# Kernel optimization log

Hardware: AMD Instinct MI355X
Metric: run time of the kernel (lower is better)

Reference implementation:

```python
import jax, jax.numpy as jnp
import numpy as np

L, D, H, W = 4, 256, 8, 20      # num_layers, hidden_dim, num_heads, walk_length
G, NPG = 512, 128               # graphs, nodes per graph (equal-size -> dense batch is a reshape)
N = G * NPG                     # 65536 nodes
E = 8 * N                       # 524288 edges (avg degree 8)
DH = D // H                     # head dim 32
FF = 2 * D                      # GPSConv MLP hidden (Linear(D, 2D))
AV, BV = 128, 8                 # padded atom / bond vocab sizes (OGB-style encoders)


def setup_inputs() -> dict:
    key = jax.random.key(0)
    ks = iter(jax.random.split(key, 40))
    nrm = lambda *s: jax.random.normal(next(ks), s, jnp.float32) * 0.02
    zeros = lambda *s: jnp.zeros(s, jnp.float32)
    ones = lambda *s: jnp.ones(s, jnp.float32)
    return dict(
        x=jax.random.randint(next(ks), (N, 9), 0, 2),
        edge_index=jax.random.randint(next(ks), (2, E), 0, N),
        edge_attr=jax.random.randint(next(ks), (E, 3), 0, 2),
        batch=jnp.repeat(jnp.arange(G), NPG),
        pe=jax.random.normal(next(ks), (N, W), jnp.float32),
        atom_emb=nrm(9, AV, D), bond_emb=nrm(3, BV, D),
        pe_w=nrm(W, D), pe_b=zeros(D),
        gine_w1=nrm(L, D, D), gine_b1=zeros(L, D),
        gine_g1=ones(L, D), gine_be1=zeros(L, D),
        gine_w2=nrm(L, D, D), gine_b2=zeros(L, D),
        attn_wqkv=nrm(L, D, 3 * D), attn_bqkv=zeros(L, 3 * D),
        attn_wo=nrm(L, D, D), attn_bo=zeros(L, D),
        n1_g=ones(L, D), n1_b=zeros(L, D),
        n2_g=ones(L, D), n2_b=zeros(L, D),
        n3_g=ones(L, D), n3_b=zeros(L, D),
        mlp_w1=nrm(L, D, FF), mlp_b1=zeros(L, FF),
        mlp_w2=nrm(L, FF, D), mlp_b2=zeros(L, D),
    )


def _bn(z, g, b):
    # BatchNorm1d over the node axis (training-mode batch statistics)
    mu = z.mean(0)
    var = z.var(0)
    return (z - mu) * jax.lax.rsqrt(var + 1e-5) * g + b


def _forward(x, edge_index, edge_attr, batch, pe, atom_emb, bond_emb, pe_w, pe_b,
             gine_w1, gine_b1, gine_g1, gine_be1, gine_w2, gine_b2,
             attn_wqkv, attn_bqkv, attn_wo, attn_bo,
             n1_g, n1_b, n2_g, n2_b, n3_g, n3_b,
             mlp_w1, mlp_b1, mlp_w2, mlp_b2):
    # AtomEncoder / BondEncoder: sum of per-column embeddings; PE fusion
    h = atom_emb[jnp.arange(9), x].sum(1) + pe @ pe_w + pe_b      # [N, D]
    ea = bond_emb[jnp.arange(3), edge_attr].sum(1)                # [E, D]
    src, dst = edge_index[0], edge_index[1]
    for l in range(L):
        # --- GINEConv: gather -> relu(x_j + e) -> scatter-add -> MLP ---
        m = jax.nn.relu(h[src] + ea)                              # [E, D]
        agg = jax.ops.segment_sum(m, dst, num_segments=N)         # [N, D]
        z = h + agg                                               # eps = 0
        z = jax.nn.relu(_bn(z @ gine_w1[l] + gine_b1[l], gine_g1[l], gine_be1[l]))
        z = jax.nn.relu(z @ gine_w2[l] + gine_b2[l])
        h_local = _bn(z + h, n1_g[l], n1_b[l])                    # residual + norm1 (dropout off)
        # --- global multi-head self-attention per graph (dense batch) ---
        xd = h.reshape(G, NPG, D)
        qkv = xd @ attn_wqkv[l] + attn_bqkv[l]                    # [G, NPG, 3D]
        q, k, v = jnp.split(qkv, 3, axis=-1)
        q = q.reshape(G, NPG, H, DH).transpose(0, 2, 1, 3)        # [G, H, NPG, DH]
        k = k.reshape(G, NPG, H, DH).transpose(0, 2, 1, 3)
        v = v.reshape(G, NPG, H, DH).transpose(0, 2, 1, 3)
        scores = jnp.einsum('ghnd,ghmd->ghnm', q, k) / jnp.sqrt(jnp.float32(DH))
        attn = jax.nn.softmax(scores, axis=-1)                    # all nodes valid (equal-size graphs)
        o = jnp.einsum('ghnm,ghmd->ghnd', attn, v)
        o = o.transpose(0, 2, 1, 3).reshape(G, NPG, D) @ attn_wo[l] + attn_bo[l]
        h_attn = _bn(o.reshape(N, D) + h, n2_g[l], n2_b[l])       # residual + norm2
        # --- combine + feed-forward MLP + norm3 ---
        out = h_local + h_attn
        out = jax.nn.relu(out @ mlp_w1[l] + mlp_b1[l]) @ mlp_w2[l] + mlp_b2[l]
        h = _bn(out, n3_g[l], n3_b[l])
    return jax.ops.segment_sum(h, batch, num_segments=G)          # global_add_pool [G, D]


def reference(x, edge_index, edge_attr, batch, pe, atom_emb, bond_emb, pe_w, pe_b,
              gine_w1, gine_b1, gine_g1, gine_be1, gine_w2, gine_b2,
              attn_wqkv, attn_bqkv, attn_wo, attn_bo,
              n1_g, n1_b, n2_g, n2_b, n3_g, n3_b,
              mlp_w1, mlp_b1, mlp_w2, mlp_b2):
    return _forward(x, edge_index, edge_attr, batch, pe, atom_emb, bond_emb, pe_w, pe_b,
                    gine_w1, gine_b1, gine_g1, gine_be1, gine_w2, gine_b2,
                    attn_wqkv, attn_bqkv, attn_wo, attn_bo,
                    n1_g, n1_b, n2_g, n2_b, n3_g, n3_b,
                    mlp_w1, mlp_b1, mlp_w2, mlp_b2)
```

## Files before the change

kernel.cpp:

```cpp
#include <hip/hip_runtime.h>
#include <stdint.h>


#define NN   65536
#define EE   524288
#define DD   256
#define LL   4
#define GG   512
#define NPGx 128
#define FFF  512

typedef __attribute__((ext_vector_type(8))) short short8;
typedef __attribute__((ext_vector_type(8))) __bf16 bf16x8;
typedef __attribute__((ext_vector_type(4))) float f32x4;

__device__ __forceinline__ float b2f(unsigned short u){
  union {unsigned int i; float f;} z; z.i = ((unsigned int)u) << 16; return z.f;
}
__device__ __forceinline__ unsigned short f2b(float f){
  union {float f; unsigned int i;} z; z.f = f;
  unsigned int r = z.i + 0x7fff + ((z.i >> 16) & 1u);
  return (unsigned short)(r >> 16);
}

__device__ __forceinline__ void gld16(void* lds, const void* g){
  __builtin_amdgcn_global_load_lds(
      (const __attribute__((address_space(1))) void*)g,
      (__attribute__((address_space(3))) void*)lds, 16, 0, 0);
}


__global__ __launch_bounds__(256) void combo_k(const float* __restrict__ be,
                                               unsigned short* __restrict__ tab){
  int c = blockIdx.x, d = threadIdx.x;
  int a0 = c & 7, a1 = (c >> 3) & 7, a2 = (c >> 6) & 7;
  tab[c*DD + d] = f2b(be[a0*DD + d] + be[(8 + a1)*DD + d] + be[(16 + a2)*DD + d]);
}

__global__ __launch_bounds__(256) void hist_k(const int* __restrict__ ei,
                                              int* __restrict__ cnt){
  for (int i = blockIdx.x*256 + threadIdx.x; i < EE; i += gridDim.x*256)
    atomicAdd(&cnt[ei[EE + i]], 1);
}

__global__ __launch_bounds__(1024) void scan_k(int* __restrict__ cnt,
                                               int* __restrict__ row_ptr){
  __shared__ int sd[1024];
  __shared__ int carry;
  int t = threadIdx.x;
  if (t == 0) carry = 0;
  __syncthreads();
  for (int base = 0; base < NN; base += 4096){
    int idx = base + t*4;
    int v0 = cnt[idx+0], v1 = cnt[idx+1], v2 = cnt[idx+2], v3 = cnt[idx+3];
    int s = v0 + v1 + v2 + v3;
    sd[t] = s; __syncthreads();
    for (int offd = 1; offd < 1024; offd <<= 1){
      int xv = (t >= offd) ? sd[t - offd] : 0;
      __syncthreads();
      sd[t] += xv;
      __syncthreads();
    }
    int excl = sd[t] - s + carry;
    row_ptr[idx+0] = excl;             cnt[idx+0] = excl;
    row_ptr[idx+1] = excl + v0;        cnt[idx+1] = excl + v0;
    row_ptr[idx+2] = excl + v0 + v1;   cnt[idx+2] = excl + v0 + v1;
    row_ptr[idx+3] = excl + v0+v1+v2;  cnt[idx+3] = excl + v0+v1+v2;
    __syncthreads();
    if (t == 0) carry += sd[1023];
    __syncthreads();
  }
  if (t == 0) row_ptr[NN] = carry;
}

__global__ __launch_bounds__(256) void fill_k(const int* __restrict__ ei,
                                              const int* __restrict__ ea,
                                              int* __restrict__ cursor,
                                              int* __restrict__ slot){
  for (int i = blockIdx.x*256 + threadIdx.x; i < EE; i += gridDim.x*256){
    int s  = ei[i];
    int dn = ei[EE + i];
    int a0 = ea[i*3+0], a1 = ea[i*3+1], a2 = ea[i*3+2];
    int cb = a0 | (a1 << 3) | (a2 << 6);
    int p = atomicAdd(&cursor[dn], 1);
    slot[p] = s | (cb << 16);
  }
}

__global__ __launch_bounds__(256) void twt_k(const float* __restrict__ w1,
                                             const float* __restrict__ w2,
                                             const float* __restrict__ wqkv,
                                             const float* __restrict__ wo,
                                             const float* __restrict__ m1,
                                             const float* __restrict__ m2,
                                             unsigned short* __restrict__ wt){
  int l = blockIdx.x / 2304;
  int r = blockIdx.x % 2304;
  const float* src; unsigned short* dst; int K, Nsrc, n;
  unsigned short* wl = wt + (size_t)l*655360;
  if (r < 256)      { src = w1  +(size_t)l*65536;  dst = wl;          K=256; Nsrc=256; n=r; }
  else if (r < 512) { src = w2  +(size_t)l*65536;  dst = wl+65536;    K=256; Nsrc=256; n=r-256; }
  else if (r < 1280){ src = wqkv+(size_t)l*196608; dst = wl+131072;   K=256; Nsrc=768; n=r-512; }
  else if (r < 1536){ src = wo  +(size_t)l*65536;  dst = wl+327680;   K=256; Nsrc=256; n=r-1280; }
  else if (r < 2048){ src = m1  +(size_t)l*131072; dst = wl+393216;   K=256; Nsrc=512; n=r-1536; }
  else              { src = m2  +(size_t)l*131072; dst = wl+524288;   K=512; Nsrc=256; n=r-2048; }
  for (int k = threadIdx.x; k < K; k += 256)
    dst[(size_t)n*K + k] = f2b(src[(size_t)k*Nsrc + n]);
}

__global__ __launch_bounds__(256) void enc_k(const int* __restrict__ x,
                                             const float* __restrict__ pe,
                                             const float* __restrict__ atom_emb,
                                             const float* __restrict__ pe_w,
                                             const float* __restrict__ pe_b,
                                             unsigned short* __restrict__ hb){
  int w = threadIdx.x >> 6, lane = threadIdx.x & 63;
  int n = blockIdx.x*4 + w;
  int d0 = lane*4;
  f32x4 acc = *(const f32x4*)(pe_b + d0);
  #pragma unroll
  for (int i = 0; i < 9; i++){
    int xi = x[n*9 + i];
    f32x4 v = *(const f32x4*)(atom_emb + (size_t)(i*128 + xi)*DD + d0);
    acc += v;
  }
  #pragma unroll
  for (int t = 0; t < 20; t++){
    float p = pe[n*20 + t];
    f32x4 v = *(const f32x4*)(pe_w + (size_t)t*DD + d0);
    acc += p * v;
  }
  ushort4 o;
  o.x = f2b(acc[0]); o.y = f2b(acc[1]); o.z = f2b(acc[2]); o.w = f2b(acc[3]);
  *(ushort4*)(hb + (size_t)n*DD + d0) = o;
}

__global__ __launch_bounds__(256) void gather_k(const unsigned short* __restrict__ hb,
                                                const int* __restrict__ row_ptr,
                                                const int* __restrict__ slot,
                                                const unsigned short* __restrict__ combo,
                                                unsigned short* __restrict__ t1){
  int w = threadIdx.x >> 6, lane = threadIdx.x & 63;
  int n = blockIdx.x*4 + w;
  int half = lane >> 5, l32 = lane & 31;
  int d0 = l32*8;
  int beg = row_ptr[n], end = row_ptr[n+1];
  float acc[8];
  #pragma unroll
  for (int u = 0; u < 8; u++) acc[u] = 0.f;
  for (int e = beg + half; e < end; e += 2){
    int s = slot[e];
    int src = s & 0xFFFF;
    int cb  = ((unsigned)s) >> 16;
    short8 hv = *(const short8*)(hb + (size_t)src*DD + d0);
    short8 cv = *(const short8*)(combo + (size_t)cb*DD + d0);
    #pragma unroll
    for (int u = 0; u < 8; u++)
      acc[u] += fmaxf(b2f((unsigned short)hv[u]) + b2f((unsigned short)cv[u]), 0.f);
  }
  #pragma unroll
  for (int u = 0; u < 8; u++) acc[u] += __shfl_xor(acc[u], 32, 64);
  if (half == 0){
    short8 hn = *(const short8*)(hb + (size_t)n*DD + d0);
    short8 o;
    #pragma unroll
    for (int u = 0; u < 8; u++) o[u] = (short)f2b(b2f((unsigned short)hn[u]) + acc[u]);
    *(short8*)(t1 + (size_t)n*DD + d0) = o;
  }
}

template<int PRO, bool RELU, bool RES, bool STATS>
__global__ __launch_bounds__(512, 2) void mgemm_k(
    const unsigned short* __restrict__ A,
    const unsigned short* __restrict__ A2,
    const unsigned short* __restrict__ Bt,
    const float* __restrict__ bias,
    const unsigned short* __restrict__ res,
    const float* __restrict__ stIn1, const float* __restrict__ gg1, const float* __restrict__ bb1,
    const float* __restrict__ stIn2, const float* __restrict__ gg2, const float* __restrict__ bb2,
    float* __restrict__ statsOut,
    unsigned short* __restrict__ C,
    int Nn, int K)
{
  __shared__ __align__(16) __bf16 SA[2][256*64];
  __shared__ __align__(16) __bf16 SB[2][256*64];
  __shared__ float cs[256], cq[256];
  __shared__ __align__(16) float scF1[256], shF1[256], scF2[256], shF2[256];

  const int tid  = threadIdx.x;
  const int wid  = tid >> 6, lane = tid & 63;
  const int row0 = blockIdx.x * 256, col0 = blockIdx.y * 256;
  const int wrr = wid >> 2, wcc = wid & 3;
  const int fr = lane & 15, fq = lane >> 4;
  const int lr8 = lane >> 3, lc8 = lane & 7;
  const int sc8 = lc8 ^ lr8;
  const int nt = K >> 6;

  if (STATS && tid < 256){ cs[tid] = 0.f; cq[tid] = 0.f; }
  if (PRO >= 1 && tid < 256){
    float mu = stIn1[tid]*(1.f/NN);
    float var = stIn1[256+tid]*(1.f/NN) - mu*mu;
    float s = rsqrtf(var + 1e-5f) * gg1[tid];
    scF1[tid] = s; shF1[tid] = bb1[tid] - mu*s;
    if (PRO == 2){
      float mu2 = stIn2[tid]*(1.f/NN);
      float va2 = stIn2[256+tid]*(1.f/NN) - mu2*mu2;
      float s2 = rsqrtf(va2 + 1e-5f) * gg2[tid];
      scF2[tid] = s2; shF2[tid] = bb2[tid] - mu2*s2;
    }
  }

  f32x4 acc[8][4];
  #pragma unroll
  for (int i = 0; i < 8; i++)
    #pragma unroll
    for (int j = 0; j < 4; j++) acc[i][j] = f32x4{0.f,0.f,0.f,0.f};

  auto stageA = [&](int buf, int kt){
    #pragma unroll
    for (int q = 0; q < 4; q++)
      gld16(&SA[buf][(wid*32 + q*8)*64],
            A + (size_t)(row0 + wid*32 + q*8 + lr8)*K + kt + sc8*8);
  };
  auto stageB = [&](int buf, int kt){
    #pragma unroll
    for (int q = 0; q < 4; q++)
      gld16(&SB[buf][(wid*32 + q*8)*64],
            Bt + (size_t)(col0 + wid*32 + q*8 + lr8)*K + kt + sc8*8);
  };

  short8 g1v[4], g4v[4];
  auto loadA = [&](int kt){
    #pragma unroll
    for (int q = 0; q < 4; q++){
      size_t rw = (size_t)(row0 + wid*32 + q*8 + lr8);
      g1v[q] = *(const short8*)(A + rw*K + kt + lc8*8);
      if (PRO == 2) g4v[q] = *(const short8*)(A2 + rw*K + kt + lc8*8);
    }
  };
  auto dswA = [&](int buf, int kt){
    const f32x4* sp1 = (const f32x4*)&scF1[kt + lc8*8];
    const f32x4* hp1 = (const f32x4*)&shF1[kt + lc8*8];
    f32x4 s1a = sp1[0], s1b = sp1[1], h1a = hp1[0], h1b = hp1[1];
    f32x4 s2a, s2b, h2a, h2b;
    if (PRO == 2){
      const f32x4* sp2 = (const f32x4*)&scF2[kt + lc8*8];
      const f32x4* hp2 = (const f32x4*)&shF2[kt + lc8*8];
      s2a = sp2[0]; s2b = sp2[1]; h2a = hp2[0]; h2b = hp2[1];
    }
    #pragma unroll
    for (int q = 0; q < 4; q++){
      short8 o;
      #pragma unroll
      for (int u = 0; u < 8; u++){
        float sc = (u < 4) ? s1a[u&3] : s1b[u&3];
        float sh = (u < 4) ? h1a[u&3] : h1b[u&3];
        float v = b2f((unsigned short)g1v[q][u]) * sc + sh;
        if (PRO == 1) v = fmaxf(v, 0.f);
        if (PRO == 2){
          float sc2 = (u < 4) ? s2a[u&3] : s2b[u&3];
          float sh2 = (u < 4) ? h2a[u&3] : h2b[u&3];
          v += b2f((unsigned short)g4v[q][u]) * sc2 + sh2;
        }
        o[u] = (short)f2b(v);
      }
      *(short8*)&SA[buf][(wid*32 + q*8 + lr8)*64 + (lc8 ^ lr8)*8] = o;
    }
  };

  if (PRO == 0){
    stageA(0, 0); stageB(0, 0);
  } else {
    loadA(0); stageB(0, 0);
    __syncthreads();
  }

  int cur = 0;
  for (int t = 0; t < nt; t++){
    if (PRO == 0){
      __syncthreads();
      if (t+1 < nt){ stageA(cur^1, (t+1)*64); stageB(cur^1, (t+1)*64); }
    } else {
      dswA(cur, t*64);
      __syncthreads();
      if (t+1 < nt){ loadA((t+1)*64); stageB(cur^1, (t+1)*64); }
    }
    #pragma unroll
    for (int ks = 0; ks < 2; ks++){
      int kc = ((ks*4 + fq) ^ (fr & 7)) * 8;
      bf16x8 a[8], b[4];
      #pragma unroll
      for (int i = 0; i < 8; i++)
        a[i] = *(const bf16x8*)&SA[cur][(wrr*128 + 16*i + fr)*64 + kc];
      #pragma unroll
      for (int j = 0; j < 4; j++)
        b[j] = *(const bf16x8*)&SB[cur][(wcc*64 + 16*j + fr)*64 + kc];
      #pragma unroll
      for (int i = 0; i < 8; i++)
        #pragma unroll
        for (int j = 0; j < 4; j++)
          acc[i][j] = __builtin_amdgcn_mfma_f32_16x16x32_bf16(a[i], b[j], acc[i][j], 0, 0, 0);
    }
    cur ^= 1;
  }

  float bj[4];
  #pragma unroll
  for (int j = 0; j < 4; j++) bj[j] = bias[col0 + wcc*64 + 16*j + fr];

  #pragma unroll
  for (int i = 0; i < 8; i++){
    #pragma unroll
    for (int j = 0; j < 4; j++){
      int col = col0 + wcc*64 + 16*j + fr;
      #pragma unroll
      for (int r = 0; r < 4; r++){
        int row = row0 + wrr*128 + 16*i + fq*4 + r;
        float y = acc[i][j][r] + bj[j];
        if constexpr (RELU) y = fmaxf(y, 0.f);
        if constexpr (RES)  y += b2f(res[(size_t)row*256 + col]);
        acc[i][j][r] = y;
        C[(size_t)row*Nn + col] = f2b(y);
      }
    }
  }

  if constexpr (STATS){
    #pragma unroll
    for (int j = 0; j < 4; j++){
      float ps = 0.f, pq = 0.f;
      #pragma unroll
      for (int i = 0; i < 8; i++)
        #pragma unroll
        for (int r = 0; r < 4; r++){ float v = acc[i][j][r]; ps += v; pq += v*v; }
      ps += __shfl_xor(ps, 16, 64); pq += __shfl_xor(pq, 16, 64);
      ps += __shfl_xor(ps, 32, 64); pq += __shfl_xor(pq, 32, 64);
      if (lane < 16){
        atomicAdd(&cs[wcc*64 + 16*j + fr], ps);
        atomicAdd(&cq[wcc*64 + 16*j + fr], pq);
      }
    }
    __syncthreads();
    if (tid < 256){
      atomicAdd(&statsOut[tid],       cs[tid]);
      atomicAdd(&statsOut[256 + tid], cq[tid]);
    }
  }
}

__global__ __launch_bounds__(256) void bnf_k(unsigned short* __restrict__ t,
                                             const float* __restrict__ st,
                                             const float* __restrict__ g,
                                             const float* __restrict__ b){
  __shared__ float sc[256], sh[256];
  int tid = threadIdx.x;
  {
    float mu  = st[tid] * (1.f/NN);
    float var = st[256+tid] * (1.f/NN) - mu*mu;
    float s   = rsqrtf(var + 1e-5f) * g[tid];
    sc[tid] = s; sh[tid] = b[tid] - mu*s;
  }
  __syncthreads();
  size_t base = ((size_t)blockIdx.x*256 + tid)*8;
  int c0 = (int)(base & 255);
  short8 v = *(const short8*)(t + base);
  short8 o;
  #pragma unroll
  for (int u = 0; u < 8; u++){
    float f = b2f((unsigned short)v[u])*sc[c0+u] + sh[c0+u];
    o[u] = (short)f2b(f);
  }
  *(short8*)(t + base) = o;
}

__global__ __launch_bounds__(64) void attn_k(const unsigned short* __restrict__ qkv,
                                             unsigned short* __restrict__ o_out){
  int g  = blockIdx.x >> 3;
  int hh = blockIdx.x & 7;
  int lane = threadIdx.x;
  int fr = lane & 15, fq = lane >> 4;
  __shared__ __align__(16) unsigned short Vt[32*136];
  __shared__ __align__(16) unsigned short P[16*128];

  const unsigned short* qb = qkv + (size_t)g*128*768 + hh*32;
  const unsigned short* kb = qb + 256;
  const unsigned short* vb = qb + 512;

  #pragma unroll
  for (int h2 = 0; h2 < 2; h2++){
    int n = lane + 64*h2;
    const short8* vr = (const short8*)(vb + (size_t)n*768);
    #pragma unroll
    for (int c = 0; c < 4; c++){
      short8 v = vr[c];
      #pragma unroll
      for (int u = 0; u < 8; u++)
        Vt[(c*8+u)*136 + n] = (unsigned short)v[u];
    }
  }
  bf16x8 bk[8];
  #pragma unroll
  for (int j = 0; j < 8; j++)
    bk[j] = *(const bf16x8*)(kb + (size_t)(16*j + fr)*768 + fq*8);
  __syncthreads();
  bf16x8 bv[4][2];
  #pragma unroll
  for (int kk = 0; kk < 4; kk++)
    #pragma unroll
    for (int j2 = 0; j2 < 2; j2++)
      bv[kk][j2] = *(const bf16x8*)&Vt[(16*j2 + fr)*136 + kk*32 + fq*8];

  const float SCALE = 0.17677669529663687f;
  for (int m0 = 0; m0 < 128; m0 += 16){
    bf16x8 aq = *(const bf16x8*)(qb + (size_t)(m0 + fr)*768 + fq*8);
    f32x4 s[8];
    #pragma unroll
    for (int j = 0; j < 8; j++)
      s[j] = __builtin_amdgcn_mfma_f32_16x16x32_bf16(aq, bk[j], f32x4{0.f,0.f,0.f,0.f}, 0, 0, 0);
    float linv[4];
    #pragma unroll
    for (int r = 0; r < 4; r++){
      float mx = s[0][r];
      #pragma unroll
      for (int j = 1; j < 8; j++) mx = fmaxf(mx, s[j][r]);
      mx = fmaxf(mx, __shfl_xor(mx, 1, 64));
      mx = fmaxf(mx, __shfl_xor(mx, 2, 64));
      mx = fmaxf(mx, __shfl_xor(mx, 4, 64));
      mx = fmaxf(mx, __shfl_xor(mx, 8, 64));
      float sum = 0.f;
      #pragma unroll
      for (int j = 0; j < 8; j++){
        float p = __expf((s[j][r] - mx) * SCALE);
        unsigned short pb = f2b(p);
        s[j][r] = b2f(pb);
        sum += s[j][r];
      }
      sum += __shfl_xor(sum, 1, 64);
      sum += __shfl_xor(sum, 2, 64);
      sum += __shfl_xor(sum, 4, 64);
      sum += __shfl_xor(sum, 8, 64);
      linv[r] = 1.f / sum;
    }
    #pragma unroll
    for (int j = 0; j < 8; j++)
      #pragma unroll
      for (int r = 0; r < 4; r++){
        int row = fq*4 + r;
        int col = (16*j + fr) ^ ((row & 7) << 3);
        P[row*128 + col] = f2b(s[j][r]);
      }
    __syncthreads();
    f32x4 o0 = {0.f,0.f,0.f,0.f}, o1 = {0.f,0.f,0.f,0.f};
    #pragma unroll
    for (int kk = 0; kk < 4; kk++){
      bf16x8 pa = *(const bf16x8*)&P[fr*128 + ((kk*32 + fq*8) ^ ((fr & 7) << 3))];
      o0 = __builtin_amdgcn_mfma_f32_16x16x32_bf16(pa, bv[kk][0], o0, 0, 0, 0);
      o1 = __builtin_amdgcn_mfma_f32_16x16x32_bf16(pa, bv[kk][1], o1, 0, 0, 0);
    }
    #pragma unroll
    for (int r = 0; r < 4; r++){
      int row = g*128 + m0 + fq*4 + r;
      unsigned short* dst = o_out + (size_t)row*DD + hh*32;
      dst[fr]      = f2b(o0[r]*linv[r]);
      dst[16 + fr] = f2b(o1[r]*linv[r]);
    }
    __syncthreads();
  }
}

__global__ __launch_bounds__(256) void pool_k(const unsigned short* __restrict__ hb,
                                              float* __restrict__ out){
  int g = blockIdx.x, d = threadIdx.x;
  float acc = 0.f;
  for (int r = 0; r < NPGx; r++) acc += b2f(hb[(size_t)(g*NPGx + r)*DD + d]);
  out[g*DD + d] = acc;
}


extern "C" void kernel_launch(void* const* d_in, const int* in_sizes, int n_in,
                              void* d_out, int out_size, void* d_ws, size_t ws_size,
                              hipStream_t stream)
{
  const int*   x         = (const int*)  d_in[0];
  const int*   ei        = (const int*)  d_in[1];
  const int*   ea        = (const int*)  d_in[2];
  const float* pe        = (const float*)d_in[4];
  const float* atom_emb  = (const float*)d_in[5];
  const float* bond_emb  = (const float*)d_in[6];
  const float* pe_w      = (const float*)d_in[7];
  const float* pe_b      = (const float*)d_in[8];
  const float* gine_w1   = (const float*)d_in[9];
  const float* gine_b1   = (const float*)d_in[10];
  const float* gine_g1   = (const float*)d_in[11];
  const float* gine_be1  = (const float*)d_in[12];
  const float* gine_w2   = (const float*)d_in[13];
  const float* gine_b2   = (const float*)d_in[14];
  const float* attn_wqkv = (const float*)d_in[15];
  const float* attn_bqkv = (const float*)d_in[16];
  const float* attn_wo   = (const float*)d_in[17];
  const float* attn_bo   = (const float*)d_in[18];
  const float* n1_g      = (const float*)d_in[19];
  const float* n1_b      = (const float*)d_in[20];
  const float* n2_g      = (const float*)d_in[21];
  const float* n2_b      = (const float*)d_in[22];
  const float* n3_g      = (const float*)d_in[23];
  const float* n3_b      = (const float*)d_in[24];
  const float* mlp_w1    = (const float*)d_in[25];
  const float* mlp_b1    = (const float*)d_in[26];
  const float* mlp_w2    = (const float*)d_in[27];
  const float* mlp_b2    = (const float*)d_in[28];
  float* out = (float*)d_out;

  char* wsp = (char*)d_ws;
  size_t off = 0;
  auto alloc = [&](size_t bytes)->void*{
    void* p = wsp + off; off += (bytes + 255) & ~(size_t)255; return p;
  };
  unsigned short* hb  = (unsigned short*)alloc((size_t)NN*DD*2);
  unsigned short* t1  = (unsigned short*)alloc((size_t)NN*DD*2);
  unsigned short* t2  = (unsigned short*)alloc((size_t)NN*DD*2);
  unsigned short* t4  = (unsigned short*)alloc((size_t)NN*DD*2);
  unsigned short* big = (unsigned short*)alloc((size_t)NN*768*2);
  unsigned short* wt  = (unsigned short*)alloc((size_t)LL*655360*2);
  unsigned short* combo = (unsigned short*)alloc((size_t)512*DD*2);
  int*   row_ptr = (int*)  alloc((size_t)(NN+1)*4);
  int*   cursor  = (int*)  alloc((size_t)NN*4);
  int*   slot    = (int*)  alloc((size_t)EE*4);
  float* stats   = (float*)alloc((size_t)LL*4*2*DD*4);
  if (off > ws_size) return;

  hipMemsetAsync(stats,  0, (size_t)LL*4*2*DD*4, stream);
  hipMemsetAsync(cursor, 0, (size_t)NN*4, stream);
  combo_k<<<512, 256, 0, stream>>>(bond_emb, combo);
  twt_k  <<<LL*2304, 256, 0, stream>>>(gine_w1, gine_w2, attn_wqkv, attn_wo,
                                       mlp_w1, mlp_w2, wt);
  hist_k <<<512, 256, 0, stream>>>(ei, cursor);
  scan_k <<<1, 1024, 0, stream>>>(cursor, row_ptr);
  fill_k <<<512, 256, 0, stream>>>(ei, ea, cursor, slot);
  enc_k  <<<NN/4, 256, 0, stream>>>(x, pe, atom_emb, pe_w, pe_b, hb);

  for (int l = 0; l < LL; l++){
    unsigned short* wl = wt + (size_t)l*655360;
    const float* b1   = gine_b1   + l*DD;
    const float* b2   = gine_b2   + l*DD;
    const float* bqkv = attn_bqkv + l*768;
    const float* bo   = attn_bo   + l*DD;
    const float* mb1  = mlp_b1    + l*FFF;
    const float* mb2  = mlp_b2    + l*DD;
    float* S0 = stats + (l*4+0)*2*DD;
    float* S1 = stats + (l*4+1)*2*DD;
    float* S2 = stats + (l*4+2)*2*DD;
    float* S3 = stats + (l*4+3)*2*DD;

    gather_k<<<NN/4, 256, 0, stream>>>(hb, row_ptr, slot, combo, t1);
    mgemm_k<0,false,false,true><<<dim3(256,1), 512, 0, stream>>>(
        t1, nullptr, wl + 0, b1, nullptr,
        nullptr,nullptr,nullptr, nullptr,nullptr,nullptr, S0, t2, 256, 256);
    mgemm_k<1,true,true,true><<<dim3(256,1), 512, 0, stream>>>(
        t2, nullptr, wl + 65536, b2, hb,
        S0, gine_g1 + l*DD, gine_be1 + l*DD, nullptr,nullptr,nullptr, S1, t1, 256, 256);
    mgemm_k<0,false,false,false><<<dim3(256,3), 512, 0, stream>>>(
        hb, nullptr, wl + 131072, bqkv, nullptr,
        nullptr,nullptr,nullptr, nullptr,nullptr,nullptr, nullptr, big, 768, 256);
    attn_k<<<GG*8, 64, 0, stream>>>(big, t2);
    mgemm_k<0,false,true,true><<<dim3(256,1), 512, 0, stream>>>(
        t2, nullptr, wl + 327680, bo, hb,
        nullptr,nullptr,nullptr, nullptr,nullptr,nullptr, S2, t4, 256, 256);
    mgemm_k<2,true,false,false><<<dim3(256,2), 512, 0, stream>>>(
        t1, t4, wl + 393216, mb1, nullptr,
        S1, n1_g + l*DD, n1_b + l*DD, S2, n2_g + l*DD, n2_b + l*DD, nullptr, big, 512, 256);
    mgemm_k<0,false,false,true><<<dim3(256,1), 512, 0, stream>>>(
        big, nullptr, wl + 524288, mb2, nullptr,
        nullptr,nullptr,nullptr, nullptr,nullptr,nullptr, S3, hb, 256, 512);
    bnf_k<<<NN*DD/2048, 256, 0, stream>>>(hb, S3, n3_g + l*DD, n3_b + l*DD);
  }
  pool_k<<<GG, 256, 0, stream>>>(hb, out);
}
```

Baseline: 1.656 ms.

## Shrink GEMM tiles to 128x256x32, tile weight transpose, batch encoder nodes

The main GEMM tile drops from 256x256 with K-step 64 to 128 rows with K-step 32. This halves LDS use and the accumulator registers, which raises occupancy (launch bounds 512,4) and doubles the grid to 512 row blocks. The price is less data reuse per block and twice as many barriers per K. The weight transpose now goes through a 64x64 LDS tile so its reads and writes are coalesced. The encoder keeps pe_w in registers and handles 8 nodes per wavefront. The stats scratch now reuses the SA buffer, and the stats atomics add a col0 offset.

New measurement: 1.654 ms. About the same (-0.1%).

```diff
diff --git a/kernel.cpp b/kernel.cpp
--- a/kernel.cpp
+++ b/kernel.cpp
@@ -94,18 +94,25 @@
                                              const float* __restrict__ m1,
                                              const float* __restrict__ m2,
                                              unsigned short* __restrict__ wt){
-  int l = blockIdx.x / 2304;
-  int r = blockIdx.x % 2304;
-  const float* src; unsigned short* dst; int K, Nsrc, n;
+  __shared__ float tile[64][65];
+  int l = blockIdx.x / 160;
+  int r = blockIdx.x % 160;
+  const float* src; unsigned short* dst; int K, Nsrc, t0;
   unsigned short* wl = wt + (size_t)l*655360;
-  if (r < 256)      { src = w1  +(size_t)l*65536;  dst = wl;          K=256; Nsrc=256; n=r; }
-  else if (r < 512) { src = w2  +(size_t)l*65536;  dst = wl+65536;    K=256; Nsrc=256; n=r-256; }
-  else if (r < 1280){ src = wqkv+(size_t)l*196608; dst = wl+131072;   K=256; Nsrc=768; n=r-512; }
-  else if (r < 1536){ src = wo  +(size_t)l*65536;  dst = wl+327680;   K=256; Nsrc=256; n=r-1280; }
-  else if (r < 2048){ src = m1  +(size_t)l*131072; dst = wl+393216;   K=256; Nsrc=512; n=r-1536; }
-  else              { src = m2  +(size_t)l*131072; dst = wl+524288;   K=512; Nsrc=256; n=r-2048; }
-  for (int k = threadIdx.x; k < K; k += 256)
-    dst[(size_t)n*K + k] = f2b(src[(size_t)k*Nsrc + n]);
+  if (r < 16)      { src = w1  +(size_t)l*65536;  dst = wl;        K=256; Nsrc=256; t0=r; }
+  else if (r < 32) { src = w2  +(size_t)l*65536;  dst = wl+65536;  K=256; Nsrc=256; t0=r-16; }
+  else if (r < 80) { src = wqkv+(size_t)l*196608; dst = wl+131072; K=256; Nsrc=768; t0=r-32; }
+  else if (r < 96) { src = wo  +(size_t)l*65536;  dst = wl+327680; K=256; Nsrc=256; t0=r-80; }
+  else if (r < 128){ src = m1  +(size_t)l*131072; dst = wl+393216; K=256; Nsrc=512; t0=r-96; }
+  else             { src = m2  +(size_t)l*131072; dst = wl+524288; K=512; Nsrc=256; t0=r-128; }
+  int nkt = K >> 6;
+  int tn = t0 / nkt, tk = t0 % nkt;
+  int rr = threadIdx.x >> 6, cc = threadIdx.x & 63;
+  for (int p = 0; p < 64; p += 4)
+    tile[p+rr][cc] = src[(size_t)(tk*64 + p + rr)*Nsrc + tn*64 + cc];
+  __syncthreads();
+  for (int p = 0; p < 64; p += 4)
+    dst[(size_t)(tn*64 + p + rr)*K + tk*64 + cc] = f2b(tile[cc][p+rr]);
 }
 
 __global__ __launch_bounds__(256) void enc_k(const int* __restrict__ x,
@@ -114,25 +121,27 @@
                                              const float* __restrict__ pe_w,
                                              const float* __restrict__ pe_b,
                                              unsigned short* __restrict__ hb){
-  int w = threadIdx.x >> 6, lane = threadIdx.x & 63;
-  int n = blockIdx.x*4 + w;
+  int wv = blockIdx.x*4 + (threadIdx.x >> 6);
+  int lane = threadIdx.x & 63;
   int d0 = lane*4;
-  f32x4 acc = *(const f32x4*)(pe_b + d0);
-  #pragma unroll
-  for (int i = 0; i < 9; i++){
-    int xi = x[n*9 + i];
-    f32x4 v = *(const f32x4*)(atom_emb + (size_t)(i*128 + xi)*DD + d0);
-    acc += v;
-  }
-  #pragma unroll
-  for (int t = 0; t < 20; t++){
-    float p = pe[n*20 + t];
-    f32x4 v = *(const f32x4*)(pe_w + (size_t)t*DD + d0);
-    acc += p * v;
-  }
-  ushort4 o;
-  o.x = f2b(acc[0]); o.y = f2b(acc[1]); o.z = f2b(acc[2]); o.w = f2b(acc[3]);
-  *(ushort4*)(hb + (size_t)n*DD + d0) = o;
+  f32x4 pw[20];
+  #pragma unroll
+  for (int t = 0; t < 20; t++) pw[t] = *(const f32x4*)(pe_w + t*DD + d0);
+  f32x4 pb = *(const f32x4*)(pe_b + d0);
+  int n0 = wv*8;
+  for (int n = n0; n < n0 + 8; n++){
+    f32x4 acc = pb;
+    #pragma unroll
+    for (int i = 0; i < 9; i++){
+      int xi = x[n*9 + i];
+      acc += *(const f32x4*)(atom_emb + (size_t)(i*128 + xi)*DD + d0);
+    }
+    #pragma unroll
+    for (int t = 0; t < 20; t++) acc += pe[n*20 + t] * pw[t];
+    ushort4 o;
+    o.x = f2b(acc[0]); o.y = f2b(acc[1]); o.z = f2b(acc[2]); o.w = f2b(acc[3]);
+    *(ushort4*)(hb + (size_t)n*DD + d0) = o;
+  }
 }
 
 __global__ __launch_bounds__(256) void gather_k(const unsigned short* __restrict__ hb,
@@ -170,7 +179,7 @@
 }
 
 template<int PRO, bool RELU, bool RES, bool STATS>
-__global__ __launch_bounds__(512, 2) void mgemm_k(
+__global__ __launch_bounds__(512, 4) void mgemm_k(
     const unsigned short* __restrict__ A,
     const unsigned short* __restrict__ A2,
     const unsigned short* __restrict__ Bt,
@@ -182,21 +191,19 @@
     unsigned short* __restrict__ C,
     int Nn, int K)
 {
-  __shared__ __align__(16) __bf16 SA[2][256*64];
-  __shared__ __align__(16) __bf16 SB[2][256*64];
-  __shared__ float cs[256], cq[256];
+  __shared__ __align__(16) __bf16 SA[2][128*32];
+  __shared__ __align__(16) __bf16 SB[2][256*32];
   __shared__ __align__(16) float scF1[256], shF1[256], scF2[256], shF2[256];
 
   const int tid  = threadIdx.x;
   const int wid  = tid >> 6, lane = tid & 63;
-  const int row0 = blockIdx.x * 256, col0 = blockIdx.y * 256;
+  const int row0 = blockIdx.x * 128, col0 = blockIdx.y * 256;
   const int wrr = wid >> 2, wcc = wid & 3;
   const int fr = lane & 15, fq = lane >> 4;
-  const int lr8 = lane >> 3, lc8 = lane & 7;
-  const int sc8 = lc8 ^ lr8;
-  const int nt = K >> 6;
-
-  if (STATS && tid < 256){ cs[tid] = 0.f; cq[tid] = 0.f; }
+  const int srow = tid >> 2, sch = tid & 3;
+  const int swc = sch ^ (srow & 3);
+  const int nt = K >> 5;
+
   if (PRO >= 1 && tid < 256){
     float mu = stIn1[tid]*(1.f/NN);
     float var = stIn1[256+tid]*(1.f/NN) - mu*mu;
@@ -210,62 +217,55 @@
     }
   }
 
-  f32x4 acc[8][4];
-  #pragma unroll
-  for (int i = 0; i < 8; i++)
+  f32x4 acc[4][4];
+  #pragma unroll
+  for (int i = 0; i < 4; i++)
     #pragma unroll
     for (int j = 0; j < 4; j++) acc[i][j] = f32x4{0.f,0.f,0.f,0.f};
 
   auto stageA = [&](int buf, int kt){
-    #pragma unroll
-    for (int q = 0; q < 4; q++)
-      gld16(&SA[buf][(wid*32 + q*8)*64],
-            A + (size_t)(row0 + wid*32 + q*8 + lr8)*K + kt + sc8*8);
+    gld16(&SA[buf][(wid*16)*32],
+          A + (size_t)(row0 + srow)*K + kt + swc*8);
   };
   auto stageB = [&](int buf, int kt){
     #pragma unroll
-    for (int q = 0; q < 4; q++)
-      gld16(&SB[buf][(wid*32 + q*8)*64],
-            Bt + (size_t)(col0 + wid*32 + q*8 + lr8)*K + kt + sc8*8);
+    for (int rr = 0; rr < 2; rr++)
+      gld16(&SB[buf][(wid*16 + rr*128)*32],
+            Bt + (size_t)(col0 + srow + rr*128)*K + kt + swc*8);
   };
 
-  short8 g1v[4], g4v[4];
+  short8 g1v, g4v;
   auto loadA = [&](int kt){
-    #pragma unroll
-    for (int q = 0; q < 4; q++){
-      size_t rw = (size_t)(row0 + wid*32 + q*8 + lr8);
-      g1v[q] = *(const short8*)(A + rw*K + kt + lc8*8);
-      if (PRO == 2) g4v[q] = *(const short8*)(A2 + rw*K + kt + lc8*8);
-    }
+    g1v = *(const short8*)(A + (size_t)(row0 + srow)*K + kt + sch*8);
+    if (PRO == 2) g4v = *(const short8*)(A2 + (size_t)(row0 + srow)*K + kt + sch*8);
   };
   auto dswA = [&](int buf, int kt){
-    const f32x4* sp1 = (const f32x4*)&scF1[kt + lc8*8];
-    const f32x4* hp1 = (const f32x4*)&shF1[kt + lc8*8];
-    f32x4 s1a = sp1[0], s1b = sp1[1], h1a = hp1[0], h1b = hp1[1];
+    f32x4 s1a = *(const f32x4*)&scF1[kt + sch*8];
+    f32x4 s1b = *(const f32x4*)&scF1[kt + sch*8 + 4];
+    f32x4 h1a = *(const f32x4*)&shF1[kt + sch*8];
+    f32x4 h1b = *(const f32x4*)&shF1[kt + sch*8 + 4];
     f32x4 s2a, s2b, h2a, h2b;
     if (PRO == 2){
-      const f32x4* sp2 = (const f32x4*)&scF2[kt + lc8*8];
-      const f32x4* hp2 = (const f32x4*)&shF2[kt + lc8*8];
-      s2a = sp2[0]; s2b = sp2[1]; h2a = hp2[0]; h2b = hp2[1];
-    }
-    #pragma unroll
-    for (int q = 0; q < 4; q++){
-      short8 o;
-      #pragma unroll
-      for (int u = 0; u < 8; u++){
-        float sc = (u < 4) ? s1a[u&3] : s1b[u&3];
-        float sh = (u < 4) ? h1a[u&3] : h1b[u&3];
-        float v = b2f((unsigned short)g1v[q][u]) * sc + sh;
-        if (PRO == 1) v = fmaxf(v, 0.f);
-        if (PRO == 2){
-          float sc2 = (u < 4) ? s2a[u&3] : s2b[u&3];
-          float sh2 = (u < 4) ? h2a[u&3] : h2b[u&3];
-          v += b2f((unsigned short)g4v[q][u]) * sc2 + sh2;
-        }
-        o[u] = (short)f2b(v);
+      s2a = *(const f32x4*)&scF2[kt + sch*8];
+      s2b = *(const f32x4*)&scF2[kt + sch*8 + 4];
+      h2a = *(const f32x4*)&shF2[kt + sch*8];
+      h2b = *(const f32x4*)&shF2[kt + sch*8 + 4];
+    }
+    short8 o;
+    #pragma unroll
+    for (int u = 0; u < 8; u++){
+      float sc = (u < 4) ? s1a[u&3] : s1b[u&3];
+      float sh = (u < 4) ? h1a[u&3] : h1b[u&3];
+      float v = b2f((unsigned short)g1v[u]) * sc + sh;
+      if (PRO == 1) v = fmaxf(v, 0.f);
+      if (PRO == 2){
+        float sc2 = (u < 4) ? s2a[u&3] : s2b[u&3];
+        float sh2 = (u < 4) ? h2a[u&3] : h2b[u&3];
+        v += b2f((unsigned short)g4v[u]) * sc2 + sh2;
       }
-      *(short8*)&SA[buf][(wid*32 + q*8 + lr8)*64 + (lc8 ^ lr8)*8] = o;
-    }
+      o[u] = (short)f2b(v);
+    }
+    *(short8*)&SA[buf][srow*32 + swc*8] = o;
   };
 
   if (PRO == 0){
@@ -279,24 +279,23 @@
   for (int t = 0; t < nt; t++){
     if (PRO == 0){
       __syncthreads();
-      if (t+1 < nt){ stageA(cur^1, (t+1)*64); stageB(cur^1, (t+1)*64); }
+      if (t+1 < nt){ stageA(cur^1, (t+1)*32); stageB(cur^1, (t+1)*32); }
     } else {
-      dswA(cur, t*64);
+      dswA(cur, t*32);
       __syncthreads();
-      if (t+1 < nt){ loadA((t+1)*64); stageB(cur^1, (t+1)*64); }
-    }
-    #pragma unroll
-    for (int ks = 0; ks < 2; ks++){
-      int kc = ((ks*4 + fq) ^ (fr & 7)) * 8;
-      bf16x8 a[8], b[4];
-      #pragma unroll
-      for (int i = 0; i < 8; i++)
-        a[i] = *(const bf16x8*)&SA[cur][(wrr*128 + 16*i + fr)*64 + kc];
+      if (t+1 < nt){ loadA((t+1)*32); stageB(cur^1, (t+1)*32); }
+    }
+    {
+      int kc = (fq ^ (fr & 3)) * 8;
+      bf16x8 a[4], b[4];
+      #pragma unroll
+      for (int i = 0; i < 4; i++)
+        a[i] = *(const bf16x8*)&SA[cur][(wrr*64 + 16*i + fr)*32 + kc];
       #pragma unroll
       for (int j = 0; j < 4; j++)
-        b[j] = *(const bf16x8*)&SB[cur][(wcc*64 + 16*j + fr)*64 + kc];
-      #pragma unroll
-      for (int i = 0; i < 8; i++)
+        b[j] = *(const bf16x8*)&SB[cur][(wcc*64 + 16*j + fr)*32 + kc];
+      #pragma unroll
+      for (int i = 0; i < 4; i++)
         #pragma unroll
         for (int j = 0; j < 4; j++)
           acc[i][j] = __builtin_amdgcn_mfma_f32_16x16x32_bf16(a[i], b[j], acc[i][j], 0, 0, 0);
@@ -309,13 +308,13 @@
   for (int j = 0; j < 4; j++) bj[j] = bias[col0 + wcc*64 + 16*j + fr];
 
   #pragma unroll
-  for (int i = 0; i < 8; i++){
+  for (int i = 0; i < 4; i++){
     #pragma unroll
     for (int j = 0; j < 4; j++){
       int col = col0 + wcc*64 + 16*j + fr;
       #pragma unroll
       for (int r = 0; r < 4; r++){
-        int row = row0 + wrr*128 + 16*i + fq*4 + r;
+        int row = row0 + wrr*64 + 16*i + fq*4 + r;
         float y = acc[i][j][r] + bj[j];
         if constexpr (RELU) y = fmaxf(y, 0.f);
         if constexpr (RES)  y += b2f(res[(size_t)row*256 + col]);
@@ -326,24 +325,29 @@
   }
 
   if constexpr (STATS){
+    float* csA = (float*)&SA[0][0];
+    float* cqA = csA + 256;
+    __syncthreads();
+    if (tid < 256){ csA[tid] = 0.f; cqA[tid] = 0.f; }
+    __syncthreads();
     #pragma unroll
     for (int j = 0; j < 4; j++){
       float ps = 0.f, pq = 0.f;
       #pragma unroll
-      for (int i = 0; i < 8; i++)
+      for (int i = 0; i < 4; i++)
         #pragma unroll
         for (int r = 0; r < 4; r++){ float v = acc[i][j][r]; ps += v; pq += v*v; }
       ps += __shfl_xor(ps, 16, 64); pq += __shfl_xor(pq, 16, 64);
       ps += __shfl_xor(ps, 32, 64); pq += __shfl_xor(pq, 32, 64);
       if (lane < 16){
-        atomicAdd(&cs[wcc*64 + 16*j + fr], ps);
-        atomicAdd(&cq[wcc*64 + 16*j + fr], pq);
+        atomicAdd(&csA[wcc*64 + 16*j + fr], ps);
+        atomicAdd(&cqA[wcc*64 + 16*j + fr], pq);
       }
     }
     __syncthreads();
     if (tid < 256){
-      atomicAdd(&statsOut[tid],       cs[tid]);
-      atomicAdd(&statsOut[256 + tid], cq[tid]);
+      atomicAdd(&statsOut[col0 + tid],       csA[tid]);
+      atomicAdd(&statsOut[256 + col0 + tid], cqA[tid]);
     }
   }
 }
@@ -532,12 +536,12 @@
   hipMemsetAsync(stats,  0, (size_t)LL*4*2*DD*4, stream);
   hipMemsetAsync(cursor, 0, (size_t)NN*4, stream);
   combo_k<<<512, 256, 0, stream>>>(bond_emb, combo);
-  twt_k  <<<LL*2304, 256, 0, stream>>>(gine_w1, gine_w2, attn_wqkv, attn_wo,
-                                       mlp_w1, mlp_w2, wt);
+  twt_k  <<<LL*160, 256, 0, stream>>>(gine_w1, gine_w2, attn_wqkv, attn_wo,
+                                      mlp_w1, mlp_w2, wt);
   hist_k <<<512, 256, 0, stream>>>(ei, cursor);
   scan_k <<<1, 1024, 0, stream>>>(cursor, row_ptr);
   fill_k <<<512, 256, 0, stream>>>(ei, ea, cursor, slot);
-  enc_k  <<<NN/4, 256, 0, stream>>>(x, pe, atom_emb, pe_w, pe_b, hb);
+  enc_k  <<<2048, 256, 0, stream>>>(x, pe, atom_emb, pe_w, pe_b, hb);
 
   for (int l = 0; l < LL; l++){
     unsigned short* wl = wt + (size_t)l*655360;
@@ -553,23 +557,23 @@
     float* S3 = stats + (l*4+3)*2*DD;
 
     gather_k<<<NN/4, 256, 0, stream>>>(hb, row_ptr, slot, combo, t1);
-    mgemm_k<0,false,false,true><<<dim3(256,1), 512, 0, stream>>>(
+    mgemm_k<0,false,false,true><<<dim3(512,1), 512, 0, stream>>>(
         t1, nullptr, wl + 0, b1, nullptr,
         nullptr,nullptr,nullptr, nullptr,nullptr,nullptr, S0, t2, 256, 256);
-    mgemm_k<1,true,true,true><<<dim3(256,1), 512, 0, stream>>>(
+    mgemm_k<1,true,true,true><<<dim3(512,1), 512, 0, stream>>>(
         t2, nullptr, wl + 65536, b2, hb,
         S0, gine_g1 + l*DD, gine_be1 + l*DD, nullptr,nullptr,nullptr, S1, t1, 256, 256);
-    mgemm_k<0,false,false,false><<<dim3(256,3), 512, 0, stream>>>(
+    mgemm_k<0,false,false,false><<<dim3(512,3), 512, 0, stream>>>(
         hb, nullptr, wl + 131072, bqkv, nullptr,
         nullptr,nullptr,nullptr, nullptr,nullptr,nullptr, nullptr, big, 768, 256);
     attn_k<<<GG*8, 64, 0, stream>>>(big, t2);
-    mgemm_k<0,false,true,true><<<dim3(256,1), 512, 0, stream>>>(
+    mgemm_k<0,false,true,true><<<dim3(512,1), 512, 0, stream>>>(
         t2, nullptr, wl + 327680, bo, hb,
         nullptr,nullptr,nullptr, nullptr,nullptr,nullptr, S2, t4, 256, 256);
-    mgemm_k<2,true,false,false><<<dim3(256,2), 512, 0, stream>>>(
+    mgemm_k<2,true,false,false><<<dim3(512,2), 512, 0, stream>>>(
         t1, t4, wl + 393216, mb1, nullptr,
         S1, n1_g + l*DD, n1_b + l*DD, S2, n2_g + l*DD, n2_b + l*DD, nullptr, big, 512, 256);
-    mgemm_k<0,false,false,true><<<dim3(256,1), 512, 0, stream>>>(
+    mgemm_k<0,false,false,true><<<dim3(512,1), 512, 0, stream>>>(
         big, nullptr, wl + 524288, mb2, nullptr,
         nullptr,nullptr,nullptr, nullptr,nullptr,nullptr, S3, hb, 256, 512);
     bnf_k<<<NN*DD/2048, 256, 0, stream>>>(hb, S3, n3_g + l*DD, n3_b + l*DD);
```
